# Kernel optimization log

Hardware: AMD Instinct MI355X
Metric: run time of the kernel (lower is better)

The kernel has to match this reference:

```python
import jax, jax.numpy as jnp
import numpy as np

N_NODES = 50000
N_EDGES = 400000
N_GRAPHS = 64
EMB = 64
H = 128
EPS = 1e-5


def _prelu(x, a):
    return jnp.where(x > 0, x, a * x)


def _batchnorm(x, gamma, beta):
    mu = x.mean(0)
    var = x.var(0)
    return gamma * (x - mu) * jax.lax.rsqrt(var + EPS) + beta


def _sage_layer(xs, W_self, W_neigh, b, a, gamma, beta, src, dst):
    # xs: list of 3 [N, Din]; params stacked over the 3 relations
    outs = []
    for i in range(3):
        x = xs[i]
        msg = x[src[i]]                                   # [E, Din] neighbor gather
        nsum = jax.ops.segment_sum(msg, dst[i], num_segments=N_NODES)
        deg = jax.ops.segment_sum(jnp.ones((src.shape[1], 1), x.dtype), dst[i], num_segments=N_NODES)
        nmean = nsum / jnp.maximum(deg, 1.0)              # zero-degree -> 0 (DGL mean reduce)
        out = x @ W_self[i] + nmean @ W_neigh[i] + b[i]
        out = _prelu(out, a[i])                           # PReLU(h_feats)
        out = _batchnorm(out, gamma[i], beta[i])          # BatchNorm1d over nodes
        outs.append(out)
    return outs


def setup_inputs() -> dict:
    key = jax.random.key(0)
    ks = jax.random.split(key, 24)
    f32 = jnp.float32
    s = 0.05
    inp = {
        'h_idx': jax.random.randint(ks[0], (N_NODES,), 0, 257),
        'p_idx': jax.random.randint(ks[1], (N_NODES,), 0, 257),
        'hp_idx': jax.random.randint(ks[2], (N_NODES,), 0, 257),
        'src': jax.random.randint(ks[3], (3, N_EDGES), 0, N_NODES),
        'dst': jax.random.randint(ks[4], (3, N_EDGES), 0, N_NODES),
        'seg': jnp.sort(jax.random.randint(ks[5], (3, N_NODES), 0, N_GRAPHS), axis=1),
        'emb_h': jax.random.normal(ks[6], (257, EMB), f32) * s,
        'emb_p': jax.random.normal(ks[7], (257, EMB), f32) * s,
        'emb_hp': jax.random.normal(ks[8], (257, EMB), f32) * s,
        # layer 1 (in = EMB)
        'W1_self': jax.random.normal(ks[9], (3, EMB, H), f32) * s,
        'W1_neigh': jax.random.normal(ks[10], (3, EMB, H), f32) * s,
        'b1': jnp.zeros((3, H), f32),
        'a1': jnp.full((3, H), 0.25, f32),
        'gamma1': jnp.ones((3, H), f32),
        'beta1': jnp.zeros((3, H), f32),
        # layers 2-4 (in = H)
        'W_self': jax.random.normal(ks[11], (3, 3, H, H), f32) * s,
        'W_neigh': jax.random.normal(ks[12], (3, 3, H, H), f32) * s,
        'b': jnp.zeros((3, 3, H), f32),
        'a': jnp.full((3, 3, H), 0.25, f32),
        'gamma': jnp.ones((3, 3, H), f32),
        'beta': jnp.zeros((3, 3, H), f32),
    }
    return inp


def reference(h_idx, p_idx, hp_idx, src, dst, seg,
              emb_h, emb_p, emb_hp,
              W1_self, W1_neigh, b1, a1, gamma1, beta1,
              W_self, W_neigh, b, a, gamma, beta):
    xs = [emb_h[h_idx], emb_p[p_idx], emb_hp[hp_idx]]      # embedding lookups
    h1 = _sage_layer(xs, W1_self, W1_neigh, b1, a1, gamma1, beta1, src, dst)
    h2 = _sage_layer(h1, W_self[0], W_neigh[0], b[0], a[0], gamma[0], beta[0], src, dst)
    h3 = _sage_layer(h2, W_self[1], W_neigh[1], b[1], a[1], gamma[1], beta[1], src, dst)
    h4 = _sage_layer(h3, W_self[2], W_neigh[2], b[2], a[2], gamma[2], beta[2], src, dst)
    vecs = []
    for i in range(3):
        hcat = jnp.concatenate((h1[i], h2[i], h3[i], h4[i]), axis=1)   # [N, 4H]
        gsum = jax.ops.segment_sum(hcat, seg[i], num_segments=N_GRAPHS)
        cnt = jax.ops.segment_sum(jnp.ones((N_NODES, 1), hcat.dtype), seg[i], num_segments=N_GRAPHS)
        vecs.append(gsum / jnp.maximum(cnt, 1.0))                      # mean_nodes
    return jnp.concatenate(vecs, axis=1)                               # [B, 12H]
```

## Files before the change

kernel.cpp:

```cpp
#include <hip/hip_runtime.h>

#define N_NODES 50000
#define N_EDGES 400000
#define N_GRAPHS 64
#define EMB 64
#define H 128
#define EPS 1e-5f

#define NCH2 49
#define NSLA 48

typedef __attribute__((ext_vector_type(8))) short bf16x8;
typedef __attribute__((ext_vector_type(4))) float f32x4;

__device__ __forceinline__ unsigned short f2b(float f) {
    unsigned int u = __builtin_bit_cast(unsigned int, f);
    unsigned int r = (u + 0x7fff + ((u >> 16) & 1)) >> 16;
    return (unsigned short)r;
}


__global__ void count_deg_kernel(const int* __restrict__ dst, int* __restrict__ deg) {
    int rel = blockIdx.y;
    int e = blockIdx.x * 256 + threadIdx.x;
    if (e < N_EDGES) atomicAdd(&deg[rel * N_NODES + dst[rel * N_EDGES + e]], 1);
}

__global__ void scan_kernel(const int* __restrict__ deg, int* __restrict__ row_ptr,
                            int* __restrict__ cur, int* __restrict__ gcur) {
    int rel = blockIdx.x;
    const int* d = deg + rel * N_NODES;
    int* rp = row_ptr + rel * (N_NODES + 1);
    int* cu = cur + rel * N_NODES;
    __shared__ int sm[1024];
    __shared__ int carry;
    if (threadIdx.x == 0) carry = 0;
    __syncthreads();
    for (int base = 0; base < N_NODES; base += 4096) {
        int i0 = base + (int)threadIdx.x * 4;
        int v[4];
        int s = 0;
#pragma unroll
        for (int k = 0; k < 4; k++) { v[k] = (i0 + k < N_NODES) ? d[i0 + k] : 0; s += v[k]; }
        sm[threadIdx.x] = s;
        __syncthreads();
        for (int off = 1; off < 1024; off <<= 1) {
            int t = (threadIdx.x >= off) ? sm[threadIdx.x - off] : 0;
            __syncthreads();
            sm[threadIdx.x] += t;
            __syncthreads();
        }
        int run = carry + sm[threadIdx.x] - s;
#pragma unroll
        for (int k = 0; k < 4; k++) {
            int i = i0 + k;
            if (i < N_NODES) {
                rp[i] = run;
                cu[i] = run;
                if ((i & 1023) == 0) gcur[rel * NCH2 + (i >> 10)] = run;
            }
            run += v[k];
        }
        __syncthreads();
        if (threadIdx.x == 1023) carry += sm[1023];
        __syncthreads();
    }
    if (threadIdx.x == 0) rp[N_NODES] = carry;
}

__global__ __launch_bounds__(256) void partA_kernel(
        const int* __restrict__ src, const int* __restrict__ dst,
        int* __restrict__ gcur, unsigned long long* __restrict__ chunkbuf) {
    int rel = blockIdx.y;
    const int* ds = dst + (size_t)rel * N_EDGES;
    const int* ss = src + (size_t)rel * N_EDGES;
    unsigned long long* cb = chunkbuf + (size_t)rel * N_EDGES;
    __shared__ int cnt[NCH2];
    __shared__ int lcur[NCH2];
    int tid = threadIdx.x;
    if (tid < NCH2) cnt[tid] = 0;
    __syncthreads();
    for (int e = blockIdx.x * 256 + tid; e < N_EDGES; e += NSLA * 256)
        atomicAdd(&cnt[ds[e] >> 10], 1);
    __syncthreads();
    if (tid < NCH2) lcur[tid] = atomicAdd(&gcur[rel * NCH2 + tid], cnt[tid]);
    __syncthreads();
    for (int e = blockIdx.x * 256 + tid; e < N_EDGES; e += NSLA * 256) {
        int dn = ds[e], sn = ss[e];
        int idx = atomicAdd(&lcur[dn >> 10], 1);
        cb[idx] = ((unsigned long long)(unsigned)sn << 32) | (unsigned)dn;
    }
}

__global__ __launch_bounds__(256) void fillB_kernel(
        const int* __restrict__ row_ptr, const unsigned long long* __restrict__ chunkbuf,
        int* __restrict__ cur, int* __restrict__ edge_src) {
    int rel = blockIdx.y;
    int c = blockIdx.x >> 1, half = blockIdx.x & 1;
    const int* rp = row_ptr + rel * (N_NODES + 1);
    int lo = rp[c << 10];
    int hiN = min((c + 1) << 10, N_NODES);
    int hi = rp[hiN];
    const unsigned long long* cb = chunkbuf + (size_t)rel * N_EDGES;
    int* cu = cur + rel * N_NODES;
    int* es = edge_src + (size_t)rel * N_EDGES;
    for (int i = lo + half + 2 * (int)threadIdx.x; i < hi; i += 2 * 256) {
        unsigned long long pr = cb[i];
        int dn = (int)(pr & 0xffffffffu);
        int sn = (int)(pr >> 32);
        int pos = atomicAdd(&cu[dn], 1);
        es[pos] = sn;
    }
}

__global__ void sort_adj_kernel(const int* __restrict__ row_ptr, int* __restrict__ edge_src) {
    int i = blockIdx.x * 256 + threadIdx.x;
    if (i >= 3 * N_NODES) return;
    int rel = i / N_NODES, n = i - rel * N_NODES;
    const int* rp = row_ptr + rel * (N_NODES + 1);
    int* es = edge_src + rel * N_EDGES;
    int s0 = rp[n], s1 = rp[n + 1];
    for (int a = s0 + 1; a < s1; a++) {
        int key = es[a];
        int b = a - 1;
        while (b >= s0 && es[b] > key) { es[b + 1] = es[b]; b--; }
        es[b + 1] = key;
    }
}


__global__ void prep_init_kernel(const float* __restrict__ W1self, const float* __restrict__ W1neigh,
                                 unsigned short* __restrict__ Wbt1,
                                 const float* __restrict__ emb_h, const float* __restrict__ emb_p,
                                 const float* __restrict__ emb_hp,
                                 unsigned short* __restrict__ emb_bf) {
    if (blockIdx.x < 192) {
        int idx = blockIdx.x * 256 + threadIdx.x;
        int rel = idx / (H * 128), rem = idx % (H * 128);
        int c = rem / 128, k = rem % 128;
        float v = (k < 64) ? W1self[((size_t)rel * 64 + k) * H + c]
                           : W1neigh[((size_t)rel * 64 + (k - 64)) * H + c];
        Wbt1[idx] = f2b(v);
    } else {
        int i = (blockIdx.x - 192) * 256 + threadIdx.x;
        if (i >= 3 * 257 * EMB / 8) return;
        int rel = i / (257 * EMB / 8), j = i % (257 * EMB / 8);
        const float* emb = rel == 0 ? emb_h : (rel == 1 ? emb_p : emb_hp);
        const float* e = emb + (size_t)j * 8;
        unsigned short o[8];
#pragma unroll
        for (int k = 0; k < 8; k++) o[k] = f2b(e[k]);
        *(uint4*)&emb_bf[(size_t)rel * 257 * EMB + (size_t)j * 8] = *(uint4*)o;
    }
}


__global__ __launch_bounds__(256) void aggregate1_kernel(
        const int* __restrict__ h_idx, const int* __restrict__ p_idx,
        const int* __restrict__ hp_idx,
        const unsigned short* __restrict__ emb_bf,
        const int* __restrict__ row_ptr, const int* __restrict__ edge_src,
        unsigned short* __restrict__ nmean) {
    const int TPN = 8;
    int rel = blockIdx.y;
    int node = blockIdx.x * 32 + threadIdx.x / TPN;
    int c8 = (threadIdx.x % TPN) * 8;
    if (node >= N_NODES) return;
    const int* idxarr = rel == 0 ? h_idx : (rel == 1 ? p_idx : hp_idx);
    const unsigned short* emb = emb_bf + (size_t)rel * 257 * EMB;
    const int* rp = row_ptr + rel * (N_NODES + 1);
    const int* es = edge_src + rel * N_EDGES;
    int s0 = rp[node], s1 = rp[node + 1];
    float acc[8];
#pragma unroll
    for (int j = 0; j < 8; j++) acc[j] = 0.f;

#define ACCUM(V)                                                                      \
    {                                                                                 \
        unsigned int w[4] = {(V).x, (V).y, (V).z, (V).w};                             \
        _Pragma("unroll") for (int j = 0; j < 4; j++) {                               \
            acc[2 * j] += __builtin_bit_cast(float, w[j] << 16);                      \
            acc[2 * j + 1] += __builtin_bit_cast(float, w[j] & 0xffff0000u);          \
        }                                                                             \
    }

    int e = s0;
    for (; e + 4 <= s1; e += 4) {
        int i0 = idxarr[es[e]], i1 = idxarr[es[e + 1]];
        int i2 = idxarr[es[e + 2]], i3 = idxarr[es[e + 3]];
        uint4 v0 = *(const uint4*)&emb[(size_t)i0 * EMB + c8];
        uint4 v1 = *(const uint4*)&emb[(size_t)i1 * EMB + c8];
        uint4 v2 = *(const uint4*)&emb[(size_t)i2 * EMB + c8];
        uint4 v3 = *(const uint4*)&emb[(size_t)i3 * EMB + c8];
        ACCUM(v0) ACCUM(v1) ACCUM(v2) ACCUM(v3)
    }
    for (; e < s1; e++) {
        uint4 v0 = *(const uint4*)&emb[(size_t)idxarr[es[e]] * EMB + c8];
        ACCUM(v0)
    }
    int deg = s1 - s0;
    float inv = 1.f / (float)max(deg, 1);
    unsigned short o[8];
#pragma unroll
    for (int j = 0; j < 8; j++)
        o[j] = (deg > 0) ? f2b(acc[j] * inv) : (unsigned short)0;
    *(uint4*)&nmean[((size_t)rel * N_NODES + node) * EMB + c8] = *(uint4*)o;
}


template <bool FOLD>
__global__ __launch_bounds__(256) void aggregate_kernel(
        const unsigned short* __restrict__ x,
        const int* __restrict__ row_ptr, const int* __restrict__ edge_src,
        const float* __restrict__ st,
        unsigned short* __restrict__ nmean) {
    const int TPN = 16;
    int rel = blockIdx.y;
    int c8 = (threadIdx.x % TPN) * 8;
    int nloc = threadIdx.x / TPN;
    const int* rp = row_ptr + rel * (N_NODES + 1);
    const int* es = edge_src + rel * N_EDGES;
    const unsigned short* xr = x + (size_t)rel * N_NODES * H;

    float sj[8], tj[8];
    if (FOLD) {
#pragma unroll
        for (int j = 0; j < 8; j++) {
            sj[j] = st[rel * 2 * H + c8 + j];
            tj[j] = st[rel * 2 * H + H + c8 + j];
        }
    }

#pragma unroll
    for (int batch = 0; batch < 6; batch++) {
        int node = blockIdx.x * 96 + batch * 16 + nloc;
        if (node >= N_NODES) continue;
        int s0 = rp[node], s1 = rp[node + 1];
        float acc[8];
#pragma unroll
        for (int j = 0; j < 8; j++) acc[j] = 0.f;
        int e = s0;
        for (; e + 4 <= s1; e += 4) {
            int i0 = es[e], i1 = es[e + 1], i2 = es[e + 2], i3 = es[e + 3];
            uint4 v0 = *(const uint4*)&xr[(size_t)i0 * H + c8];
            uint4 v1 = *(const uint4*)&xr[(size_t)i1 * H + c8];
            uint4 v2 = *(const uint4*)&xr[(size_t)i2 * H + c8];
            uint4 v3 = *(const uint4*)&xr[(size_t)i3 * H + c8];
            ACCUM(v0) ACCUM(v1) ACCUM(v2) ACCUM(v3)
        }
        for (; e < s1; e++) {
            uint4 v0 = *(const uint4*)&xr[(size_t)es[e] * H + c8];
            ACCUM(v0)
        }
        int deg = s1 - s0;
        float inv = 1.f / (float)max(deg, 1);
        unsigned short o[8];
#pragma unroll
        for (int j = 0; j < 8; j++) {
            float m = acc[j] * inv;
            if (FOLD) m = sj[j] * m + tj[j];
            o[j] = (deg > 0) ? f2b(m) : (unsigned short)0;
        }
        *(uint4*)&nmean[((size_t)rel * N_NODES + node) * H + c8] = *(uint4*)o;
    }
#undef ACCUM
}


template <int KX, bool G1, bool STORE>
__global__ __launch_bounds__(512) void gemm_kernel(
        const unsigned short* __restrict__ x,
        const unsigned short* __restrict__ nmean,
        const unsigned short* __restrict__ Wbt,
        const float* __restrict__ bias,
        const float* __restrict__ alpha,
        unsigned short* __restrict__ out,
        float* __restrict__ stats,
        const int* __restrict__ seg_all,
        float* __restrict__ gout,
        int layer,
        const unsigned short* __restrict__ embt,
        const int* __restrict__ h_idx, const int* __restrict__ p_idx,
        const int* __restrict__ hp_idx) {
    const int KTOT = 2 * KX;
    int rel = blockIdx.y;
    int row0 = blockIdx.x * 128;
    const unsigned short* xr = x + (size_t)rel * N_NODES * KX;
    const unsigned short* nm = nmean + (size_t)rel * N_NODES * KX;
    const unsigned short* W = Wbt + (size_t)rel * H * KTOT;
    unsigned short* o = out + (size_t)rel * N_NODES * H;

    __shared__ __align__(16) short At[128][40];
    __shared__ __align__(16) short Bt[128][40];

    int tid = threadIdx.x;
    int lane = tid & 63;
    int wave = tid >> 6;
    int wr = wave >> 2;
    int wcq = wave & 3;
    int l15 = lane & 15;
    int koff = (lane >> 4) * 8;

    f32x4 acc[4][2];
#pragma unroll
    for (int m = 0; m < 4; m++)
#pragma unroll
        for (int n = 0; n < 2; n++) acc[m][n] = (f32x4){0.f, 0.f, 0.f, 0.f};

    int seg = tid & 3;
    int rloc = tid >> 2;

    int nid0 = 0;
    if (G1) {
        const int* idxarr = rel == 0 ? h_idx : (rel == 1 ? p_idx : hp_idx);
        if (row0 + rloc < N_NODES) nid0 = idxarr[row0 + rloc];
    }
    const unsigned short* et = G1 ? (embt + (size_t)rel * 257 * EMB) : nullptr;

    for (int kc = 0; kc < KTOT; kc += 32) {
        const bool selfh = kc < KX;
        const unsigned short* Asrc = selfh ? xr : nm;
        int kb = selfh ? kc : kc - KX;
        {
            int gr = row0 + rloc;
            uint4 v = make_uint4(0u, 0u, 0u, 0u);
            if (gr < N_NODES) {
                if (G1 && selfh) v = *(const uint4*)&et[(size_t)nid0 * EMB + kb + seg * 8];
                else             v = *(const uint4*)&Asrc[(size_t)gr * KX + kb + seg * 8];
            }
            *(uint4*)&At[rloc][seg * 8] = v;
            *(uint4*)&Bt[rloc][seg * 8] = *(const uint4*)&W[(size_t)rloc * KTOT + kc + seg * 8];
        }
        __syncthreads();
        bf16x8 a[4], b[2];
#pragma unroll
        for (int m = 0; m < 4; m++) a[m] = *(const bf16x8*)&At[wr * 64 + m * 16 + l15][koff];
#pragma unroll
        for (int n = 0; n < 2; n++) b[n] = *(const bf16x8*)&Bt[wcq * 32 + n * 16 + l15][koff];
#pragma unroll
        for (int m = 0; m < 4; m++)
#pragma unroll
            for (int n = 0; n < 2; n++)
                acc[m][n] = __builtin_amdgcn_mfma_f32_16x16x32_bf16(a[m], b[n], acc[m][n], 0, 0, 0);
        __syncthreads();
    }

    float bs[2], as_[2];
#pragma unroll
    for (int n = 0; n < 2; n++) {
        int col = wcq * 32 + n * 16 + l15;
        bs[n] = bias[rel * H + col];
        as_[n] = alpha[rel * H + col];
    }
    const int* sg = seg_all + rel * N_NODES;
    float csum[2] = {0.f, 0.f}, cssq[2] = {0.f, 0.f};
    int curg = -1;
    float run[2] = {0.f, 0.f};
    int rbase = row0 + wr * 64 + (lane >> 4) * 4;
#pragma unroll
    for (int m = 0; m < 4; m++) {
#pragma unroll
        for (int j = 0; j < 4; j++) {
            int r = rbase + m * 16 + j;
            if (r >= N_NODES) continue;
            int g = sg[r];
            if (g != curg) {
                if (curg >= 0) {
                    float* ob = gout + (size_t)curg * (3 * 4 * H) + rel * (4 * H) + layer * H + wcq * 32 + l15;
#pragma unroll
                    for (int n = 0; n < 2; n++) { atomicAdd(ob + n * 16, run[n]); run[n] = 0.f; }
                }
                curg = g;
            }
#pragma unroll
            for (int n = 0; n < 2; n++) {
                float v = acc[m][n][j] + bs[n];
                v = v > 0.f ? v : as_[n] * v;
                if (STORE) o[(size_t)r * H + wcq * 32 + n * 16 + l15] = f2b(v);
                csum[n] += v;
                cssq[n] += v * v;
                run[n] += v;
            }
        }
    }
    if (curg >= 0) {
        float* ob = gout + (size_t)curg * (3 * 4 * H) + rel * (4 * H) + layer * H + wcq * 32 + l15;
#pragma unroll
        for (int n = 0; n < 2; n++) atomicAdd(ob + n * 16, run[n]);
    }
    __syncthreads();
    float* smS = (float*)&At[0][0];
    float* smQ = (float*)&Bt[0][0];
    int contrib = wr * 4 + (lane >> 4);
#pragma unroll
    for (int n = 0; n < 2; n++) {
        int col = wcq * 32 + n * 16 + l15;
        smS[col * 8 + contrib] = csum[n];
        smQ[col * 8 + contrib] = cssq[n];
    }
    __syncthreads();
    if (tid < 128) {
        float s = 0.f, q = 0.f;
#pragma unroll
        for (int i = 0; i < 8; i++) { s += smS[tid * 8 + i]; q += smQ[tid * 8 + i]; }
        atomicAdd(&stats[rel * 256 + tid], s);
        atomicAdd(&stats[rel * 256 + 128 + tid], q);
    }
}


__global__ void finalize_kernel(float* __restrict__ stats,
                                const float* __restrict__ gamma, const float* __restrict__ beta,
                                float* __restrict__ st) {
    int rel = blockIdx.x, c = threadIdx.x;
    const float invN = 1.f / N_NODES;
    float mu = stats[rel * 256 + c] * invN;
    float var = stats[rel * 256 + 128 + c] * invN - mu * mu;
    float s = gamma[rel * H + c] * rsqrtf(var + EPS);
    st[rel * 2 * H + c] = s;
    st[rel * 2 * H + H + c] = beta[rel * H + c] - mu * s;
    stats[rel * 256 + c] = 0.f;
    stats[rel * 256 + 128 + c] = 0.f;
}


__global__ void prep_kernel(const float* __restrict__ Wself, const float* __restrict__ Wneigh,
                            const float* __restrict__ b, const float* __restrict__ st,
                            unsigned short* __restrict__ Wbt, float* __restrict__ biasp) {
    if (blockIdx.x < 384) {
        int idx = blockIdx.x * 256 + threadIdx.x;
        int rel = idx / (H * 256), rem = idx % (H * 256);
        int c = rem / 256, k = rem % 256;
        float v;
        if (k < 128) v = st[rel * 2 * H + k] * Wself[((size_t)rel * H + k) * H + c];
        else         v = Wneigh[((size_t)rel * H + (k - 128)) * H + c];
        Wbt[idx] = f2b(v);
    } else if (threadIdx.x < H) {
        int rel = blockIdx.x - 384, c = threadIdx.x;
        const float* t = st + rel * 2 * H + H;
        float s = b[rel * H + c];
        for (int k = 0; k < H; k++) s += t[k] * Wself[((size_t)rel * H + k) * H + c];
        biasp[rel * H + c] = s;
    }
}


__global__ void scale_out_kernel(float* __restrict__ out, const int* __restrict__ seg,
                                 const float* __restrict__ st_all) {
    int i = blockIdx.x * 256 + threadIdx.x;
    if (i >= N_GRAPHS * 3 * 4 * H) return;
    int g = i / (3 * 4 * H), k = i % (3 * 4 * H);
    int rel = k / (4 * H), rem = k % (4 * H), layer = rem / H, c = rem % H;
    const int* sg = seg + rel * N_NODES;
    int lo = 0, hi = N_NODES;
    while (lo < hi) { int m = (lo + hi) >> 1; if (sg[m] < g) lo = m + 1; else hi = m; }
    int start = lo;
    hi = N_NODES;
    while (lo < hi) { int m = (lo + hi) >> 1; if (sg[m] <= g) lo = m + 1; else hi = m; }
    int cnt = lo - start;
    float mean = out[i] / (float)max(cnt, 1);
    const float* st = st_all + ((size_t)layer * 3 + rel) * 2 * H;
    out[i] = st[c] * mean + st[H + c];
}


extern "C" void kernel_launch(void* const* d_in, const int* in_sizes, int n_in,
                              void* d_out, int out_size, void* d_ws, size_t ws_size,
                              hipStream_t stream) {
    const int* h_idx = (const int*)d_in[0];
    const int* p_idx = (const int*)d_in[1];
    const int* hp_idx = (const int*)d_in[2];
    const int* src = (const int*)d_in[3];
    const int* dst = (const int*)d_in[4];
    const int* seg = (const int*)d_in[5];
    const float* emb_h = (const float*)d_in[6];
    const float* emb_p = (const float*)d_in[7];
    const float* emb_hp = (const float*)d_in[8];
    const float* W1_self = (const float*)d_in[9];
    const float* W1_neigh = (const float*)d_in[10];
    const float* b1 = (const float*)d_in[11];
    const float* a1 = (const float*)d_in[12];
    const float* gamma1 = (const float*)d_in[13];
    const float* beta1 = (const float*)d_in[14];
    const float* W_self = (const float*)d_in[15];
    const float* W_neigh = (const float*)d_in[16];
    const float* b = (const float*)d_in[17];
    const float* a = (const float*)d_in[18];
    const float* gamma = (const float*)d_in[19];
    const float* beta = (const float*)d_in[20];
    float* out = (float*)d_out;

    char* p = (char*)d_ws;
    unsigned short* hpA = (unsigned short*)p; p += (size_t)3 * N_NODES * H * 2;
    unsigned short* hpB = (unsigned short*)p; p += (size_t)3 * N_NODES * H * 2;
    unsigned short* Wbt1 = (unsigned short*)p; p += (size_t)3 * H * 128 * 2;
    unsigned short* Wbt = (unsigned short*)p; p += (size_t)3 * H * 256 * 2;
    unsigned short* emb_bf = (unsigned short*)p; p += (size_t)3 * 257 * EMB * 2;
    float* biasp = (float*)p; p += 3 * H * sizeof(float);
    float* st_all = (float*)p; p += 4 * 3 * 2 * H * sizeof(float);
    float* stats = (float*)p; p += 3 * 256 * sizeof(float);
    int* deg = (int*)p; p += (size_t)3 * N_NODES * 4;
    int* row_ptr = (int*)p; p += (size_t)3 * (N_NODES + 1) * 4;
    int* cur = (int*)p; p += (size_t)3 * N_NODES * 4;
    int* gcur = (int*)p; p += (size_t)3 * NCH2 * 4;
    int* edge_src = (int*)p; p += (size_t)3 * N_EDGES * 4;
    unsigned long long* chunkbuf = (unsigned long long*)p; p += (size_t)3 * N_EDGES * 8;

    hipMemsetAsync(out, 0, (size_t)N_GRAPHS * 3 * 4 * H * sizeof(float), stream);
    hipMemsetAsync(stats, 0, 3 * 256 * 4, stream);

    hipMemsetAsync(deg, 0, (size_t)3 * N_NODES * 4, stream);
    dim3 eb((N_EDGES + 255) / 256, 3);
    count_deg_kernel<<<eb, 256, 0, stream>>>(dst, deg);
    scan_kernel<<<3, 1024, 0, stream>>>(deg, row_ptr, cur, gcur);
    partA_kernel<<<dim3(NSLA, 3), 256, 0, stream>>>(src, dst, gcur, chunkbuf);
    fillB_kernel<<<dim3(2 * NCH2, 3), 256, 0, stream>>>(row_ptr, chunkbuf, cur, edge_src);
    sort_adj_kernel<<<(3 * N_NODES + 255) / 256, 256, 0, stream>>>(row_ptr, edge_src);

    prep_init_kernel<<<217, 256, 0, stream>>>(W1_self, W1_neigh, Wbt1,
                                              emb_h, emb_p, emb_hp, emb_bf);

    dim3 gemm_grid((N_NODES + 127) / 128, 3);
    dim3 agg_grid((N_NODES + 95) / 96, 3);

    aggregate1_kernel<<<dim3((N_NODES + 31) / 32, 3), 256, 0, stream>>>(
        h_idx, p_idx, hp_idx, emb_bf, row_ptr, edge_src, hpB);
    gemm_kernel<64, true, true><<<gemm_grid, 512, 0, stream>>>(
        emb_bf , hpB, Wbt1, b1, a1, hpA, stats, seg, out, 0,
        emb_bf, h_idx, p_idx, hp_idx);
    finalize_kernel<<<3, H, 0, stream>>>(stats, gamma1, beta1, st_all);

    unsigned short* xin = hpA;
    unsigned short* xout = hpB;
    for (int l = 0; l < 3; l++) {
        const float* st_prev = st_all + (size_t)l * 3 * 2 * H;
        prep_kernel<<<387, 256, 0, stream>>>(
            W_self + (size_t)l * 3 * H * H, W_neigh + (size_t)l * 3 * H * H,
            b + (size_t)l * 3 * H, st_prev, Wbt, biasp);
        aggregate_kernel<true><<<agg_grid, 256, 0, stream>>>(
            xin, row_ptr, edge_src, st_prev, xout);
        if (l < 2)
            gemm_kernel<128, false, true><<<gemm_grid, 512, 0, stream>>>(
                xin, xout, Wbt, biasp, a + (size_t)l * 3 * H, xout, stats, seg, out, l + 1,
                nullptr, nullptr, nullptr, nullptr);
        else
            gemm_kernel<128, false, false><<<gemm_grid, 512, 0, stream>>>(
                xin, xout, Wbt, biasp, a + (size_t)l * 3 * H, xout, stats, seg, out, l + 1,
                nullptr, nullptr, nullptr, nullptr);
        finalize_kernel<<<3, H, 0, stream>>>(
            stats, gamma + (size_t)l * 3 * H, beta + (size_t)l * 3 * H,
            st_all + (size_t)(l + 1) * 3 * 2 * H);
        unsigned short* t = xin; xin = xout; xout = t;
    }

    scale_out_kernel<<<(N_GRAPHS * 3 * 4 * H + 255) / 256, 256, 0, stream>>>(out, seg, st_all);
}
```

Measured before the change: 655.8 us.

## Load A fragments directly from global and stage full weight half in LDS

The GEMM kernel no longer stages A tiles through shared memory. Each lane now loads its MFMA A fragments straight from global memory (or from the embedding table in layer 1). The weight matrix is staged in LDS once per half (self / neighbor) instead of once per 32-wide K chunk, which removes most of the per-chunk __syncthreads barriers. The tradeoff is that A rows are read redundantly across the four column waves, with less coalesced global access, and the LDS buffer grows to KX+8 columns.

```diff
diff --git a/kernel.cpp b/kernel.cpp
--- a/kernel.cpp
+++ b/kernel.cpp
@@ -290,8 +290,7 @@
     const unsigned short* W = Wbt + (size_t)rel * H * KTOT;
     unsigned short* o = out + (size_t)rel * N_NODES * H;
 
-    __shared__ __align__(16) short At[128][40];
-    __shared__ __align__(16) short Bt[128][40];
+    __shared__ __align__(16) short Bl[128][KX + 8];
 
     int tid = threadIdx.x;
     int lane = tid & 63;
@@ -307,42 +306,50 @@
 #pragma unroll
         for (int n = 0; n < 2; n++) acc[m][n] = (f32x4){0.f, 0.f, 0.f, 0.f};
 
-    int seg = tid & 3;
-    int rloc = tid >> 2;
-
-    int nid0 = 0;
-    if (G1) {
-        const int* idxarr = rel == 0 ? h_idx : (rel == 1 ? p_idx : hp_idx);
-        if (row0 + rloc < N_NODES) nid0 = idxarr[row0 + rloc];
+    size_t arow[4];
+    int nid[4];
+#pragma unroll
+    for (int m = 0; m < 4; m++) {
+        int r = row0 + wr * 64 + m * 16 + l15;
+        int rc = min(r, N_NODES - 1);
+        arow[m] = (size_t)rc * KX;
+        if (G1) {
+            const int* idxarr = rel == 0 ? h_idx : (rel == 1 ? p_idx : hp_idx);
+            nid[m] = idxarr[rc];
+        }
     }
     const unsigned short* et = G1 ? (embt + (size_t)rel * 257 * EMB) : nullptr;
 
-    for (int kc = 0; kc < KTOT; kc += 32) {
-        const bool selfh = kc < KX;
-        const unsigned short* Asrc = selfh ? xr : nm;
-        int kb = selfh ? kc : kc - KX;
+#pragma unroll
+    for (int ph = 0; ph < 2; ph++) {
+        __syncthreads();
         {
-            int gr = row0 + rloc;
-            uint4 v = make_uint4(0u, 0u, 0u, 0u);
-            if (gr < N_NODES) {
-                if (G1 && selfh) v = *(const uint4*)&et[(size_t)nid0 * EMB + kb + seg * 8];
-                else             v = *(const uint4*)&Asrc[(size_t)gr * KX + kb + seg * 8];
+            int c = tid >> 2;
+            int s8 = (tid & 3) * 8;
+#pragma unroll
+            for (int q = 0; q < KX; q += 32)
+                *(uint4*)&Bl[c][q + s8] = *(const uint4*)&W[(size_t)c * KTOT + ph * KX + q + s8];
+        }
+        __syncthreads();
+        const unsigned short* As = (ph == 0) ? xr : nm;
+        for (int kc = 0; kc < KX; kc += 32) {
+            bf16x8 a[4], b[2];
+#pragma unroll
+            for (int m = 0; m < 4; m++) {
+                if (G1 && ph == 0)
+                    a[m] = *(const bf16x8*)&et[(size_t)nid[m] * EMB + kc + koff];
+                else
+                    a[m] = *(const bf16x8*)&As[arow[m] + kc + koff];
             }
-            *(uint4*)&At[rloc][seg * 8] = v;
-            *(uint4*)&Bt[rloc][seg * 8] = *(const uint4*)&W[(size_t)rloc * KTOT + kc + seg * 8];
-        }
-        __syncthreads();
-        bf16x8 a[4], b[2];
-#pragma unroll
-        for (int m = 0; m < 4; m++) a[m] = *(const bf16x8*)&At[wr * 64 + m * 16 + l15][koff];
-#pragma unroll
-        for (int n = 0; n < 2; n++) b[n] = *(const bf16x8*)&Bt[wcq * 32 + n * 16 + l15][koff];
-#pragma unroll
-        for (int m = 0; m < 4; m++)
 #pragma unroll
             for (int n = 0; n < 2; n++)
-                acc[m][n] = __builtin_amdgcn_mfma_f32_16x16x32_bf16(a[m], b[n], acc[m][n], 0, 0, 0);
-        __syncthreads();
+                b[n] = *(const bf16x8*)&Bl[wcq * 32 + n * 16 + l15][kc + koff];
+#pragma unroll
+            for (int m = 0; m < 4; m++)
+#pragma unroll
+                for (int n = 0; n < 2; n++)
+                    acc[m][n] = __builtin_amdgcn_mfma_f32_16x16x32_bf16(a[m], b[n], acc[m][n], 0, 0, 0);
+        }
     }
 
     float bs[2], as_[2];
@@ -389,8 +396,8 @@
         for (int n = 0; n < 2; n++) atomicAdd(ob + n * 16, run[n]);
     }
     __syncthreads();
-    float* smS = (float*)&At[0][0];
-    float* smQ = (float*)&Bt[0][0];
+    float* smS = (float*)&Bl[0][0];
+    float* smQ = smS + 1024;
     int contrib = wr * 4 + (lane >> 4);
 #pragma unroll
     for (int n = 0; n < 2; n++) {
```

After: 718.0 us. 1.09x slower.
